# Performance work log

Hardware: AMD Instinct MI355X
Metric: run time of the kernel (lower is better)

## Reference

```python
import jax, jax.numpy as jnp
import numpy as np

D = 48; N_IN = 8192; K = 24; RADIUS = 0.033
C_HID = 86; C_IN = 5; EMB = 16; MODES = 6; PAD = 6; N_LAYERS = 4
EPS = 1e-5


def _pos_embed(x):
    # neuraloperator PositionalEmbedding: scalar -> EMB channels (cos || sin)
    half = EMB // 2
    freqs = (1.0 / 10000.0) ** (jnp.arange(half, dtype=x.dtype) / half)
    ang = x[:, None] * freqs[None, :]
    return jnp.concatenate([jnp.cos(ang), jnp.sin(ang)], axis=-1)


def _gelu(x):
    return jax.nn.gelu(x, approximate=False)


def _conv1x1(h, w, b):
    return jnp.einsum('oi,ixyz->oxyz', w, h) + b[:, None, None, None]


def _group_norm(h, w, b):
    # GroupNorm(num_groups=1) on a batch-1 [C,X,Y,Z] tensor
    mu = jnp.mean(h)
    var = jnp.var(h)
    hn = (h - mu) * jax.lax.rsqrt(var + EPS)
    return hn * w[:, None, None, None] + b[:, None, None, None]


def _spectral_conv(h, wr, wi):
    S = h.shape[1]
    Xf = jnp.fft.rfftn(h, axes=(1, 2, 3))  # [C,S,S,S//2+1] complex64
    W = wr + 1j * wi                        # [4,C,C,m,m,m]
    out = jnp.zeros_like(Xf)
    m = MODES
    sls = (slice(0, m), slice(-m, None))
    c = 0
    for a in range(2):
        for b in range(2):
            blk = Xf[:, sls[a], sls[b], :m]
            res = jnp.einsum('ixyz,ioxyz->oxyz', blk, W[c])
            out = out.at[:, sls[a], sls[b], :m].set(res)
            c += 1
    return jnp.fft.irfftn(out, s=(S, S, S), axes=(1, 2, 3))


def _forward(x_in, x_out, df, w_lift, b_lift, spec_wr, spec_wi,
             w_skip, b_skip, mlp1_w, mlp1_b, mlp2_w, mlp2_b, wms, bms,
             g1_w, g1_b, g2_w, g2_b, k1_w, k1_b, k2_w, k2_b, k3_w, k3_b,
             p1_w, p1_b, p2_w, p2_b, nb_idx, nb_mask):
    n_out = D ** 3
    x_out_embed = _pos_embed(x_out.reshape(-1)).reshape(n_out, 3 * EMB)
    feat = jnp.concatenate([df, jnp.transpose(x_out, (3, 0, 1, 2))], axis=0)  # [5,D,D,D]
    h = _conv1x1(feat, w_lift, b_lift)
    h = jnp.pad(h, ((0, 0), (0, PAD), (0, PAD), (0, PAD)))  # one-sided domain padding
    for l in range(N_LAYERS):
        skip = _conv1x1(h, w_skip[l], b_skip[l])
        hf = _group_norm(_spectral_conv(h, spec_wr[l], spec_wi[l]), g1_w[l], g1_b[l])
        h = hf + skip
        if l < N_LAYERS - 1:
            h = _gelu(h)
        mskip = _conv1x1(h, wms[l], bms[l])
        hm = _conv1x1(_gelu(_conv1x1(h, mlp1_w[l], mlp1_b[l])), mlp2_w[l], mlp2_b[l])
        hm = _group_norm(hm, g2_w[l], g2_b[l])
        h = hm + mskip
        if l < N_LAYERS - 1:
            h = _gelu(h)
    h = h[:, :D, :D, :D]
    f_y = h.reshape(C_HID, n_out).T  # [n_out, C_HID]
    x_in_embed = _pos_embed(x_in.reshape(-1)).reshape(N_IN, 3 * EMB)
    # GNO: gather -> kernel MLP -> elementwise (linear kernel) -> mean scatter-reduce
    y_g = x_out_embed[nb_idx]                                        # [N,K,48]
    q_g = jnp.broadcast_to(x_in_embed[:, None, :], (N_IN, K, 3 * EMB))
    kin = jnp.concatenate([y_g, q_g], axis=-1)                       # [N,K,96]
    k = _gelu(kin @ k1_w.T + k1_b)
    k = _gelu(k @ k2_w.T + k2_b)
    k = k @ k3_w.T + k3_b                                            # [N,K,C_HID]
    f_g = f_y[nb_idx]                                                # [N,K,C_HID]
    mask = nb_mask[..., None].astype(k.dtype)
    num = jnp.sum(k * f_g * mask, axis=1)
    den = jnp.maximum(jnp.sum(nb_mask, axis=1), 1).astype(k.dtype)[:, None]
    out = num / den
    out = _gelu(out @ p1_w.T + p1_b)
    return out @ p2_w.T + p2_b                                       # [N,1]


def setup_inputs():
    rng = np.random.default_rng(0)
    lin = np.linspace(0.0, 1.0, D, dtype=np.float32)
    gx, gy, gz = np.meshgrid(lin, lin, lin, indexing='ij')
    x_out = np.stack([gx, gy, gz], axis=-1)                          # [D,D,D,3]
    x_in = rng.random((N_IN, 3)).astype(np.float32)
    # --- host-side ball-query neighbor search (regular grid, radius=RADIUS) ---
    spacing = 1.0 / (D - 1)
    rc = int(np.ceil(RADIUS / spacing))
    offs = np.arange(-rc, rc + 1)
    oi, oj, ok = np.meshgrid(offs, offs, offs, indexing='ij')
    offsets = np.stack([oi.ravel(), oj.ravel(), ok.ravel()], axis=-1)
    base = np.floor(x_in / spacing + 0.5).astype(np.int64)
    cand = base[:, None, :] + offsets[None, :, :]
    ok_v = np.all((cand >= 0) & (cand < D), axis=-1)
    cand = np.clip(cand, 0, D - 1)
    d2 = np.sum((cand.astype(np.float32) * spacing - x_in[:, None, :]) ** 2, axis=-1)
    inball = ok_v & (d2 <= RADIUS ** 2)
    order = np.argsort(~inball, axis=1, kind='stable')[:, :K]
    flat = (cand[..., 0] * D + cand[..., 1]) * D + cand[..., 2]
    nb_idx = np.take_along_axis(flat, order, axis=1).astype(np.int32)
    nb_mask = np.take_along_axis(inball, order, axis=1)

    def lw(o, i):
        return jnp.asarray((rng.standard_normal((o, i)) / np.sqrt(i)).astype(np.float32))

    def slw(n, o, i):
        return jnp.asarray((rng.standard_normal((n, o, i)) / np.sqrt(i)).astype(np.float32))

    m = MODES
    ss = 1.0 / C_HID
    spec_wr = jnp.asarray((rng.standard_normal((N_LAYERS, 4, C_HID, C_HID, m, m, m)) * ss).astype(np.float32))
    spec_wi = jnp.asarray((rng.standard_normal((N_LAYERS, 4, C_HID, C_HID, m, m, m)) * ss).astype(np.float32))
    zC = jnp.zeros((N_LAYERS, C_HID), dtype=jnp.float32)
    oC = jnp.ones((N_LAYERS, C_HID), dtype=jnp.float32)
    return dict(
        x_in=jnp.asarray(x_in), x_out=jnp.asarray(x_out),
        df=jnp.asarray(rng.standard_normal((C_IN - 3, D, D, D)).astype(np.float32)),
        nb_idx=jnp.asarray(nb_idx), nb_mask=jnp.asarray(nb_mask),
        w_lift=lw(C_HID, C_IN), b_lift=jnp.zeros(C_HID, dtype=jnp.float32),
        spec_wr=spec_wr, spec_wi=spec_wi,
        w_skip=slw(N_LAYERS, C_HID, C_HID), b_skip=zC,
        mlp1_w=slw(N_LAYERS, C_HID, C_HID), mlp1_b=zC,
        mlp2_w=slw(N_LAYERS, C_HID, C_HID), mlp2_b=zC,
        wms=slw(N_LAYERS, C_HID, C_HID), bms=zC,
        g1_w=oC, g1_b=zC, g2_w=oC, g2_b=zC,
        k1_w=lw(512, 6 * EMB), k1_b=jnp.zeros(512, dtype=jnp.float32),
        k2_w=lw(256, 512), k2_b=jnp.zeros(256, dtype=jnp.float32),
        k3_w=lw(C_HID, 256), k3_b=jnp.zeros(C_HID, dtype=jnp.float32),
        p1_w=lw(256, C_HID), p1_b=jnp.zeros(256, dtype=jnp.float32),
        p2_w=lw(1, 256), p2_b=jnp.zeros(1, dtype=jnp.float32),
    )


def reference(x_in, x_out, df, nb_idx, nb_mask, w_lift, b_lift, spec_wr, spec_wi,
              w_skip, b_skip, mlp1_w, mlp1_b, mlp2_w, mlp2_b, wms, bms,
              g1_w, g1_b, g2_w, g2_b, k1_w, k1_b, k2_w, k2_b, k3_w, k3_b,
              p1_w, p1_b, p2_w, p2_b):
    return _forward(x_in, x_out, df, w_lift, b_lift, spec_wr, spec_wi,
                    w_skip, b_skip, mlp1_w, mlp1_b, mlp2_w, mlp2_b, wms, bms,
                    g1_w, g1_b, g2_w, g2_b, k1_w, k1_b, k2_w, k2_b, k3_w, k3_b,
                    p1_w, p1_b, p2_w, p2_b, nb_idx, nb_mask)
```

## Files before the change

kernel.cpp:

```cpp
#include <hip/hip_runtime.h>
#include <math.h>

#define CH 86
#define SP 54
#define SS2 2916
#define SS3 157464
#define DG 48
#define MPAD 157568
#define RT_ROWS (CH*SS2)
#define NSLICE (CH*SP)
#define PI_F 3.14159265358979323846f
#define GN_INV (1.0/13541904.0)

static constexpr size_t A512(size_t x){ return (x + 511) & ~((size_t)511); }
static constexpr size_t HB2 = (size_t)CH*SS3*2;
static constexpr size_t HB4 = (size_t)CH*SS3*4;
static constexpr size_t AB2 = (size_t)MPAD*96*2;
static constexpr size_t XB4 = (size_t)MPAD*96*4;
static constexpr size_t FAB = (size_t)CH*SS2*6*8;
static constexpr size_t FBB = (size_t)CH*SP*12*6*8;
static constexpr size_t FCB = (size_t)CH*864*8;
static constexpr size_t OFF_HA = 0;
static constexpr size_t OFF_HS = OFF_HA + A512(HB2);
static constexpr size_t OFF_AB = OFF_HS + A512(HB4);
static constexpr size_t OFF_BB = OFF_AB + A512(AB2);
static constexpr size_t OFF_XSC= OFF_BB + A512(AB2);
static constexpr size_t OFF_FA = OFF_XSC+ A512(XB4);
static constexpr size_t OFF_FB = OFF_FA + A512(FAB);
static constexpr size_t OFF_FC = OFF_FB + A512(FBB);
static constexpr size_t OFF_FD = OFF_FC + A512(FCB);
static constexpr size_t OFF_FE = OFF_FD + A512(FCB);
static constexpr size_t OFF_ST = OFF_FE + A512(FBB);
static constexpr size_t OFF_WB = OFF_ST + 512;
static constexpr size_t OFF_P1W= OFF_WB + A512((size_t)16*96*96*2);
static constexpr size_t OFF_W1 = OFF_P1W+ A512((size_t)256*96*2);
static constexpr size_t OFF_W2 = OFF_W1 + A512((size_t)512*96*2);
static constexpr size_t OFF_W3 = OFF_W2 + A512((size_t)256*512*2);
static constexpr size_t OFF_K3 = OFF_W3 + A512((size_t)86*256*2);
static constexpr size_t OFF_Z2 = OFF_K3 + A512((size_t)196608*CH*4);
static constexpr size_t OFF_U  = OFF_Z2 + A512((size_t)98304*256*2);
static constexpr size_t OFF_H1 = OFF_U  + A512((size_t)8192*96*2);
static constexpr int    CHUNK_M = 98304;
static constexpr size_t OFF_KIN = 0;
static constexpr size_t OFF_Z1  = A512((size_t)CHUNK_M*96*2);

typedef __attribute__((ext_vector_type(8))) short bf16x8;
typedef __attribute__((ext_vector_type(4))) float f32x4;

__device__ __forceinline__ float gelu_f(float x){
  return 0.5f*x*(1.0f + erff(x*0.70710678118654752440f));
}
__device__ __forceinline__ unsigned short f2bf(float x){
  unsigned u = __float_as_uint(x);
  u += 0x7fffu + ((u>>16)&1u);
  return (unsigned short)(u>>16);
}
__device__ __forceinline__ float bf2f(unsigned short u){
  return __uint_as_float(((unsigned)u)<<16);
}

__global__ void k_zero_stats(double* st){ if (threadIdx.x < 16) st[threadIdx.x] = 0.0; }

__global__ __launch_bounds__(256) void k_f2bf(const float* __restrict__ in,
    unsigned short* __restrict__ out, int n)
{
  int i = blockIdx.x*256 + threadIdx.x;
  if (i < n) out[i] = f2bf(in[i]);
}

__global__ __launch_bounds__(256) void k_wprep(const float* __restrict__ src,
    unsigned short* __restrict__ dst, int slot)
{
  int l = blockIdx.y;
  int idx = blockIdx.x*256 + threadIdx.x;
  int n = idx/96, k = idx-96*n;
  unsigned short v = 0;
  if (n < 86 && k < 86) v = f2bf(src[(size_t)l*7396 + n*86 + k]);
  dst[(size_t)(l*4+slot)*9216 + idx] = v;
}

__global__ __launch_bounds__(256) void k_pad_w(const float* __restrict__ src,
    unsigned short* __restrict__ dst, int rows)
{
  int idx = blockIdx.x*256 + threadIdx.x;
  if (idx >= rows*96) return;
  int n = idx/96, k = idx-96*n;
  dst[idx] = (k<86)? f2bf(src[n*86+k]) : (unsigned short)0;
}

__global__ __launch_bounds__(256) void k_lift(const float* __restrict__ df,
    const float* __restrict__ wl, const float* __restrict__ bl,
    unsigned short* __restrict__ hA, unsigned short* __restrict__ Ab)
{
  __shared__ float vals[128*96];
  const int t = threadIdx.x;
  const int s0 = blockIdx.x*128;
  for(int idx=t; idx<128*96; idx+=256){
    int sl = idx/96, o = idx-96*sl;
    int s = s0+sl;
    float v = 0.f;
    if (o < 86){
      int x = s/2916, r2 = s-2916*x, y = r2/54, z = r2-54*y;
      if (x<DG && y<DG && z<DG){
        int p = (x*DG + y)*DG + z;
        v = wl[o*5]*df[p] + wl[o*5+1]*df[110592+p]
          + wl[o*5+2]*(x*(1.0f/47.0f)) + wl[o*5+3]*(y*(1.0f/47.0f))
          + wl[o*5+4]*(z*(1.0f/47.0f)) + bl[o];
      }
    }
    vals[idx] = v;
  }
  __syncthreads();
  for(int idx=t; idx<128*96; idx+=256)
    Ab[(size_t)s0*96 + idx] = f2bf(vals[idx]);
  for(int idx=t; idx<86*128; idx+=256){
    int c = idx/128, sl = idx-128*c;
    int s = s0+sl;
    if (s < SS3) hA[(size_t)c*SS3 + s] = f2bf(vals[sl*96 + c]);
  }
}

__global__ __launch_bounds__(256) void k_dft_z(const unsigned short* __restrict__ h, float* __restrict__ A)
{
  __shared__ alignas(16) float rows[64*55];
  __shared__ float twc[6*54], tws[6*54];
  const int t = threadIdx.x;
  for(int idx=t; idx<6*54; idx+=256){
    int k = idx/54, z = idx-54*k;
    int m = (k*z)%54;
    float ang = -(2.0f*PI_F/54.0f)*(float)m;
    twc[idx]=cosf(ang); tws[idx]=sinf(ang);
  }
  const int r0 = blockIdx.x*64;
  for(int idx=t; idx<64*54; idx+=256){
    int r = idx/54;
    rows[r*55 + (idx-54*r)] = (r0+r < RT_ROWS)? bf2f(h[(size_t)r0*54 + idx]) : 0.f;
  }
  __syncthreads();
  for(int oi=t; oi<768; oi+=256){
    int r = oi & 63;
    int k = (oi>>6)%6;
    int part = oi/384;
    if (r0+r < RT_ROWS){
      const float* tw = part? tws : twc;
      const float* rp = &rows[r*55];
      const float* twk = &tw[k*54];
      float acc=0.f;
      #pragma unroll 6
      for(int z=0;z<54;z++) acc += rp[z]*twk[z];
      A[((size_t)(r0+r)*6 + k)*2 + part] = acc;
    }
  }
}

__global__ __launch_bounds__(256) void k_dft_y(const float* __restrict__ A, float* __restrict__ B)
{
  __shared__ float asl[4*648];
  __shared__ float twc[12*54], tws[12*54];
  const int t = threadIdx.x;
  for(int idx=t; idx<12*54; idx+=256){
    int kyi = idx/54, y = idx-54*kyi;
    int ky = (kyi<6)? kyi : (42+kyi);
    int m = (ky*y)%54;
    float ang = -(2.0f*PI_F/54.0f)*(float)m;
    twc[idx]=cosf(ang); tws[idx]=sinf(ang);
  }
  const int s0 = blockIdx.x*4;
  for(int idx=t; idx<4*648; idx+=256){
    int sl = idx/648;
    asl[idx] = (s0+sl < NSLICE)? A[(size_t)s0*648 + idx] : 0.f;
  }
  __syncthreads();
  for(int oi=t; oi<4*72; oi+=256){
    int sl = oi/72, o = oi-72*sl;
    if (s0+sl >= NSLICE) continue;
    int kyi = o/6, kz = o-6*kyi;
    const float* base = &asl[sl*648];
    float cr=0.f, ci=0.f;
    for(int y=0;y<54;y++){
      float ar = base[(y*6+kz)*2], ai = base[(y*6+kz)*2+1];
      float tc = twc[kyi*54+y], ts = tws[kyi*54+y];
      cr += ar*tc - ai*ts;
      ci += ar*ts + ai*tc;
    }
    size_t ob = ((size_t)(s0+sl)*12 + kyi)*6 + kz;
    B[ob*2]=cr; B[ob*2+1]=ci;
  }
}

__global__ __launch_bounds__(256) void k_dft_x(const float* __restrict__ B, float* __restrict__ C)
{
  __shared__ float bsl[7776];
  __shared__ float twc[12*54], tws[12*54];
  const int t = threadIdx.x;
  const int i = blockIdx.x;
  for(int idx=t; idx<12*54; idx+=256){
    int kxi = idx/54, x = idx-54*kxi;
    int kx = (kxi<6)? kxi : (42+kxi);
    int m = (kx*x)%54;
    float ang = -(2.0f*PI_F/54.0f)*(float)m;
    twc[idx]=cosf(ang); tws[idx]=sinf(ang);
  }
  for(int idx=t; idx<7776; idx+=256) bsl[idx] = B[(size_t)i*7776 + idx];
  __syncthreads();
  for(int oi=t; oi<864; oi+=256){
    int kxi = oi/72, rest = oi-72*kxi;
    float cr=0.f, ci=0.f;
    for(int x=0;x<54;x++){
      float br = bsl[(x*72+rest)*2], bi = bsl[(x*72+rest)*2+1];
      float tc = twc[kxi*54+x], ts = tws[kxi*54+x];
      cr += br*tc - bi*ts;
      ci += br*ts + bi*tc;
    }
    int kyi = rest/6, kz = rest-6*kyi;
    int c = ((kxi>=6)?2:0) + ((kyi>=6)?1:0);
    int f = ((kxi%6)*6 + (kyi%6))*6 + kz;
    size_t ob = ((size_t)i*4 + c)*216 + f;
    C[ob*2]=cr; C[ob*2+1]=ci;
  }
}

__global__ __launch_bounds__(256) void k_mix(const float* __restrict__ C,
    const float* __restrict__ wr, const float* __restrict__ wi, float* __restrict__ D)
{
  const int f = threadIdx.x;
  if (f >= 216) return;
  const int o = blockIdx.x, c = blockIdx.y;
  const size_t wstride = (size_t)CH*216;
  const float* wrp = wr + ((size_t)c*CH*CH + o)*216 + f;
  const float* wip = wi + ((size_t)c*CH*CH + o)*216 + f;
  const float* cp  = C + ((size_t)c*216 + f)*2;
  float ar=0.f, ai=0.f;
  #pragma unroll 4
  for(int i=0;i<CH;i++){
    float cr = cp[0], cim = cp[1];
    float xr = *wrp, xi = *wip;
    ar += cr*xr - cim*xi;
    ai += cr*xi + cim*xr;
    wrp += wstride; wip += wstride;
    cp += 864*2;
  }
  int mx = f/36, my = (f/6)%6, kz = f%6;
  int kxi = mx + ((c>=2)?6:0);
  int kyi = my + ((c&1)?6:0);
  size_t ob = (((size_t)o*12 + kxi)*12 + kyi)*6 + kz;
  D[ob*2]=ar; D[ob*2+1]=ai;
}

__global__ __launch_bounds__(256) void k_idft_x(const float* __restrict__ D, float* __restrict__ E)
{
  __shared__ float dsl[1728];
  __shared__ float twc[12*54], tws[12*54];
  const int t = threadIdx.x;
  const int o = blockIdx.x;
  for(int idx=t; idx<12*54; idx+=256){
    int kxi = idx/54, x = idx-54*kxi;
    int kx = (kxi<6)? kxi : (42+kxi);
    int m = (kx*x)%54;
    float ang = (2.0f*PI_F/54.0f)*(float)m;
    twc[idx]=cosf(ang); tws[idx]=sinf(ang);
  }
  for(int idx=t; idx<1728; idx+=256) dsl[idx] = D[(size_t)o*1728 + idx];
  __syncthreads();
  for(int oi=t; oi<3888; oi+=256){
    int x = oi/72, rest = oi-72*x;
    float er=0.f, ei=0.f;
    #pragma unroll
    for(int kxi=0;kxi<12;kxi++){
      float dr = dsl[(kxi*72+rest)*2], di = dsl[(kxi*72+rest)*2+1];
      float tc = twc[kxi*54+x], ts = tws[kxi*54+x];
      er += dr*tc - di*ts;
      ei += dr*ts + di*tc;
    }
    size_t ob = (size_t)o*3888 + oi;
    E[ob*2]=er; E[ob*2+1]=ei;
  }
}

__global__ __launch_bounds__(256) void k_idft_y(const float* __restrict__ E, float* __restrict__ F)
{
  __shared__ float esl[4*144];
  __shared__ float twc[12*54], tws[12*54];
  const int t = threadIdx.x;
  for(int idx=t; idx<12*54; idx+=256){
    int kyi = idx/54, y = idx-54*kyi;
    int ky = (kyi<6)? kyi : (42+kyi);
    int m = (ky*y)%54;
    float ang = (2.0f*PI_F/54.0f)*(float)m;
    twc[idx]=cosf(ang); tws[idx]=sinf(ang);
  }
  const int s0 = blockIdx.x*4;
  for(int idx=t; idx<4*144; idx+=256){
    int sl = idx/144;
    esl[idx] = (s0+sl < NSLICE)? E[(size_t)s0*144 + idx] : 0.f;
  }
  __syncthreads();
  for(int oi=t; oi<4*324; oi+=256){
    int sl = oi/324, rest = oi-324*sl;
    if (s0+sl >= NSLICE) continue;
    int y = rest/6, kz = rest-6*y;
    const float* base = &esl[sl*144];
    float fr=0.f, fi=0.f;
    #pragma unroll
    for(int kyi=0;kyi<12;kyi++){
      float er = base[(kyi*6+kz)*2], ei = base[(kyi*6+kz)*2+1];
      float tc = twc[kyi*54+y], ts = tws[kyi*54+y];
      fr += er*tc - ei*ts;
      fi += er*ts + ei*tc;
    }
    size_t ob = ((size_t)(s0+sl)*54 + y)*6 + kz;
    F[ob*2]=fr; F[ob*2+1]=fi;
  }
}

__global__ __launch_bounds__(256) void k_idft_z(const float* __restrict__ F,
    float* __restrict__ hs, double* __restrict__ st)
{
  __shared__ float rws[64*12];
  __shared__ float twc[5*54], tws[5*54];
  __shared__ float red[8];
  const int t = threadIdx.x;
  for(int idx=t; idx<5*54; idx+=256){
    int k = idx/54 + 1, z = idx%54;
    int m = (k*z)%54;
    float ang = (2.0f*PI_F/54.0f)*(float)m;
    twc[idx]=cosf(ang); tws[idx]=sinf(ang);
  }
  const int r0 = blockIdx.x*64;
  for(int idx=t; idx<768; idx+=256){
    int r = idx/12;
    rws[idx] = (r0+r < RT_ROWS)? F[(size_t)r0*12 + idx] : 0.f;
  }
  __syncthreads();
  const float inv = 1.0f/157464.0f;
  float lsum=0.f, lsq=0.f;
  for(int oi=t; oi<64*54; oi+=256){
    int r = oi/54, z = oi-54*r;
    if (r0+r < RT_ROWS){
      const float* fr = &rws[r*12];
      float acc = fr[0];
      #pragma unroll
      for(int k=1;k<=5;k++)
        acc += 2.0f*(fr[2*k]*twc[(k-1)*54+z] - fr[2*k+1]*tws[(k-1)*54+z]);
      acc *= inv;
      hs[(size_t)r0*54 + oi] = acc;
      lsum += acc; lsq += acc*acc;
    }
  }
  #pragma unroll
  for(int off=32; off; off>>=1){
    lsum += __shfl_down(lsum, off, 64);
    lsq  += __shfl_down(lsq,  off, 64);
  }
  if ((t&63)==0){ red[(t>>6)*2]=lsum; red[(t>>6)*2+1]=lsq; }
  __syncthreads();
  if (t==0){
    double s1 = (double)red[0]+red[2]+red[4]+red[6];
    double s2 = (double)red[1]+red[3]+red[5]+red[7];
    atomicAdd(st, s1); atomicAdd(st+1, s2);
  }
}

template<int ACT1>
__global__ __launch_bounds__(256) void k_fuse3(
    const unsigned short* __restrict__ Ain, const unsigned short* __restrict__ Wl3,
    const float* __restrict__ bsk, const float* __restrict__ b1,
    const float* __restrict__ b2,
    const float* __restrict__ hS, const float* __restrict__ g1,
    const float* __restrict__ bg1, const double* __restrict__ st1,
    double* __restrict__ st2,
    unsigned short* __restrict__ Bb, float* __restrict__ Hm)
{
  __shared__ unsigned short Wl[96*96];
  __shared__ unsigned short Achunk[8*512];
  __shared__ unsigned short Tt[128*96];
  __shared__ float red[8];
  const int t = threadIdx.x, lane = t&63, w = t>>6;
  const int m0 = blockIdx.x*128;
  const int lr = lane>>2, lq = lane&3;
  const int colb = lane&15, rowq = (lane>>4)*4;
  f32x4 acc[2][6];

  for(int s=w; s<18; s+=4){
    const unsigned short* gw = Wl3 + s*512 + lane*8;
    __builtin_amdgcn_global_load_lds((const __attribute__((address_space(1))) void*)gw,
        (__attribute__((address_space(3))) void*)&Wl[s*512], 16, 0, 0);
  }
  #pragma unroll
  for(int s=0;s<2;s++)
    #pragma unroll
    for(int n=0;n<6;n++) acc[s][n] = (f32x4){0.f,0.f,0.f,0.f};
  #pragma unroll
  for(int k0=0;k0<96;k0+=32){
    __syncthreads();
    #pragma unroll
    for(int j=0;j<2;j++){
      int slot = w*2+j;
      int row = slot*16 + lr;
      const unsigned short* ga = Ain + (size_t)(m0+row)*96 + k0 + lq*8;
      __builtin_amdgcn_global_load_lds((const __attribute__((address_space(1))) void*)ga,
          (__attribute__((address_space(3))) void*)&Achunk[slot*512], 16, 0, 0);
    }
    __syncthreads();
    bf16x8 af[2], bf[6];
    #pragma unroll
    for(int s=0;s<2;s++)
      af[s] = *(const bf16x8*)&Achunk[(w*32 + s*16 + (lane&15))*32 + (lane>>4)*8];
    #pragma unroll
    for(int n=0;n<6;n++)
      bf[n] = *(const bf16x8*)&Wl[(n*16 + (lane&15))*96 + k0 + (lane>>4)*8];
    #pragma unroll
    for(int s=0;s<2;s++)
      #pragma unroll
      for(int n=0;n<6;n++)
        acc[s][n] = __builtin_amdgcn_mfma_f32_16x16x32_bf16(af[s], bf[n], acc[s][n], 0, 0, 0);
  }
  {
    double m = st1[0]*GN_INV;
    double va = st1[1]*GN_INV - m*m;
    float mu = (float)m, rs = (float)(1.0/sqrt(va + 1e-5));
    #pragma unroll
    for(int n=0;n<6;n++){
      int col = n*16 + colb;
      bool cv = (col < CH);
      float bn=0.f, gg=1.f, bb=0.f;
      if (cv){ bn = bsk[col]; gg = g1[col]; bb = bg1[col]; }
      #pragma unroll
      for(int s=0;s<2;s++){
        #pragma unroll
        for(int r=0;r<4;r++){
          int rowl = w*32 + s*16 + rowq + r;
          int row = m0 + rowl;
          float v = 0.f;
          if (cv){
            v = acc[s][n][r] + bn;
            if (row < SS3) v += (hS[(size_t)col*SS3 + row]-mu)*rs*gg + bb;
            if (ACT1) v = gelu_f(v);
          }
          unsigned short vb = f2bf(v);
          Bb[(size_t)row*96 + col] = vb;
          Tt[rowl*96 + col] = vb;
        }
      }
    }
  }

  __syncthreads();
  for(int s=w; s<18; s+=4){
    const unsigned short* gw = Wl3 + 9216 + s*512 + lane*8;
    __builtin_amdgcn_global_load_lds((const __attribute__((address_space(1))) void*)gw,
        (__attribute__((address_space(3))) void*)&Wl[s*512], 16, 0, 0);
  }
  #pragma unroll
  for(int s=0;s<2;s++)
    #pragma unroll
    for(int n=0;n<6;n++) acc[s][n] = (f32x4){0.f,0.f,0.f,0.f};
  __syncthreads();
  #pragma unroll
  for(int k0=0;k0<96;k0+=32){
    bf16x8 af[2], bf[6];
    #pragma unroll
    for(int s=0;s<2;s++)
      af[s] = *(const bf16x8*)&Tt[(w*32 + s*16 + (lane&15))*96 + k0 + (lane>>4)*8];
    #pragma unroll
    for(int n=0;n<6;n++)
      bf[n] = *(const bf16x8*)&Wl[(n*16 + (lane&15))*96 + k0 + (lane>>4)*8];
    #pragma unroll
    for(int s=0;s<2;s++)
      #pragma unroll
      for(int n=0;n<6;n++)
        acc[s][n] = __builtin_amdgcn_mfma_f32_16x16x32_bf16(af[s], bf[n], acc[s][n], 0, 0, 0);
  }
  #pragma unroll
  for(int n=0;n<6;n++){
    int col = n*16 + colb;
    bool cv = (col < CH);
    float bn = cv? b1[col] : 0.f;
    #pragma unroll
    for(int s=0;s<2;s++){
      #pragma unroll
      for(int r=0;r<4;r++){
        int rowl = w*32 + s*16 + rowq + r;
        float v = cv? gelu_f(acc[s][n][r] + bn) : 0.f;
        Tt[rowl*96 + col] = f2bf(v);
      }
    }
  }

  __syncthreads();
  for(int s=w; s<18; s+=4){
    const unsigned short* gw = Wl3 + 18432 + s*512 + lane*8;
    __builtin_amdgcn_global_load_lds((const __attribute__((address_space(1))) void*)gw,
        (__attribute__((address_space(3))) void*)&Wl[s*512], 16, 0, 0);
  }
  #pragma unroll
  for(int s=0;s<2;s++)
    #pragma unroll
    for(int n=0;n<6;n++) acc[s][n] = (f32x4){0.f,0.f,0.f,0.f};
  __syncthreads();
  #pragma unroll
  for(int k0=0;k0<96;k0+=32){
    bf16x8 af[2], bf[6];
    #pragma unroll
    for(int s=0;s<2;s++)
      af[s] = *(const bf16x8*)&Tt[(w*32 + s*16 + (lane&15))*96 + k0 + (lane>>4)*8];
    #pragma unroll
    for(int n=0;n<6;n++)
      bf[n] = *(const bf16x8*)&Wl[(n*16 + (lane&15))*96 + k0 + (lane>>4)*8];
    #pragma unroll
    for(int s=0;s<2;s++)
      #pragma unroll
      for(int n=0;n<6;n++)
        acc[s][n] = __builtin_amdgcn_mfma_f32_16x16x32_bf16(af[s], bf[n], acc[s][n], 0, 0, 0);
  }
  float lsum=0.f, lsq=0.f;
  #pragma unroll
  for(int n=0;n<6;n++){
    int col = n*16 + colb;
    bool cv = (col < CH);
    float bn = cv? b2[col] : 0.f;
    #pragma unroll
    for(int s=0;s<2;s++){
      #pragma unroll
      for(int r=0;r<4;r++){
        int row = m0 + w*32 + s*16 + rowq + r;
        float v = 0.f;
        if (cv){
          v = acc[s][n][r] + bn;
          if (row < SS3){ lsum += v; lsq += v*v; }
        }
        Hm[(size_t)row*96 + col] = v;
      }
    }
  }
  #pragma unroll
  for(int off=32; off; off>>=1){
    lsum += __shfl_down(lsum, off, 64);
    lsq  += __shfl_down(lsq,  off, 64);
  }
  if (lane==0){ red[w*2]=lsum; red[w*2+1]=lsq; }
  __syncthreads();
  if (t==0){
    double s1 = (double)red[0]+red[2]+red[4]+red[6];
    double s2 = (double)red[1]+red[3]+red[5]+red[7];
    atomicAdd(st2, s1); atomicAdd(st2+1, s2);
  }
}

template<int LAST>
__global__ __launch_bounds__(256) void k_convms(
    const unsigned short* __restrict__ Ain, const unsigned short* __restrict__ Wm,
    const float* __restrict__ bms,
    const float* __restrict__ Hm, const float* __restrict__ g2,
    const float* __restrict__ bg2, const double* __restrict__ st2,
    unsigned short* __restrict__ Ab, unsigned short* __restrict__ hA,
    float* __restrict__ FY)
{
  __shared__ unsigned short Wl[96*96];
  __shared__ unsigned short Achunk[8*512];
  const int t = threadIdx.x, lane = t&63, w = t>>6;
  const int m0 = blockIdx.x*128;
  const int lr = lane>>2, lq = lane&3;
  for(int s=w; s<18; s+=4){
    const unsigned short* gw = Wm + s*512 + lane*8;
    __builtin_amdgcn_global_load_lds((const __attribute__((address_space(1))) void*)gw,
        (__attribute__((address_space(3))) void*)&Wl[s*512], 16, 0, 0);
  }
  f32x4 acc[2][6];
  #pragma unroll
  for(int s=0;s<2;s++)
    #pragma unroll
    for(int n=0;n<6;n++) acc[s][n] = (f32x4){0.f,0.f,0.f,0.f};
  #pragma unroll
  for(int k0=0;k0<96;k0+=32){
    __syncthreads();
    #pragma unroll
    for(int j=0;j<2;j++){
      int slot = w*2+j;
      int row = slot*16 + lr;
      const unsigned short* ga = Ain + (size_t)(m0+row)*96 + k0 + lq*8;
      __builtin_amdgcn_global_load_lds((const __attribute__((address_space(1))) void*)ga,
          (__attribute__((address_space(3))) void*)&Achunk[slot*512], 16, 0, 0);
    }
    __syncthreads();
    bf16x8 af[2], bf[6];
    #pragma unroll
    for(int s=0;s<2;s++)
      af[s] = *(const bf16x8*)&Achunk[(w*32 + s*16 + (lane&15))*32 + (lane>>4)*8];
    #pragma unroll
    for(int n=0;n<6;n++)
      bf[n] = *(const bf16x8*)&Wl[(n*16 + (lane&15))*96 + k0 + (lane>>4)*8];
    #pragma unroll
    for(int s=0;s<2;s++)
      #pragma unroll
      for(int n=0;n<6;n++)
        acc[s][n] = __builtin_amdgcn_mfma_f32_16x16x32_bf16(af[s], bf[n], acc[s][n], 0, 0, 0);
  }
  double m = st2[0]*GN_INV;
  double va = st2[1]*GN_INV - m*m;
  float mu = (float)m, rs = (float)(1.0/sqrt(va + 1e-5));
  const int colb = lane&15, rowq = (lane>>4)*4;
  #pragma unroll
  for(int n=0;n<6;n++){
    int col = n*16 + colb;
    bool cv = (col < CH);
    float bn=0.f, gg=1.f, bb=0.f;
    if (cv){ bn = bms[col]; gg = g2[col]; bb = bg2[col]; }
    #pragma unroll
    for(int s=0;s<2;s++){
      #pragma unroll
      for(int r=0;r<4;r++){
        int row = m0 + w*32 + s*16 + rowq + r;
        float v = 0.f;
        if (cv){
          v = acc[s][n][r] + bn + (Hm[(size_t)row*96 + col]-mu)*rs*gg + bb;
          if (!LAST) v = gelu_f(v);
        }
        if (LAST){
          FY[(size_t)row*96 + col] = v;
        } else {
          Ab[(size_t)row*96 + col] = f2bf(v);
          if (cv && row < SS3) hA[(size_t)col*SS3 + row] = f2bf(v);
        }
      }
    }
  }
}

__global__ __launch_bounds__(256) void k_build_kin(const float* __restrict__ x_in,
    const int* __restrict__ nb_idx, unsigned short* __restrict__ kin, int pair0)
{
  int gidx = blockIdx.x*256 + threadIdx.x;
  int lp = gidx/96, col = gidx - lp*96;
  int pair = pair0 + lp;
  int qi = pair/24;
  int cc = col; bool isq = false;
  if (cc >= 48){ cc -= 48; isq = true; }
  int ci = cc>>4, e = cc&15;
  int f = e&7; bool is_sin = (e>=8);
  float coord;
  if (isq){
    coord = x_in[qi*3 + ci];
  } else {
    int pt = nb_idx[pair];
    int gcoord;
    if (ci==0) gcoord = pt/2304;
    else if (ci==1) gcoord = (pt/48)%48;
    else gcoord = pt%48;
    coord = gcoord*(1.0f/47.0f);
  }
  float freq = exp2f(-(float)f * 1.66096404744368117f);
  float ang = coord*freq;
  kin[gidx] = f2bf(is_sin ? sinf(ang) : cosf(ang));
}

template<int ACT, int OUT_BF16>
__global__ __launch_bounds__(256,2) void k_gemm_mfma(
    const unsigned short* __restrict__ A, const unsigned short* __restrict__ B,
    const float* __restrict__ bias, void* __restrict__ Cout,
    int M, int N, int K)
{
  __shared__ unsigned short As[128*32];
  __shared__ unsigned short Bs[128*32];
  const int t = threadIdx.x;
  const int lane = t & 63, w = t >> 6;
  const int wm = w >> 1, wn = w & 1;
  const int m0 = blockIdx.x*128, n0 = blockIdx.y*128;
  const int lr = lane >> 2, lq = lane & 3;
  f32x4 acc[4][4];
  #pragma unroll
  for(int s=0;s<4;s++)
    #pragma unroll
    for(int n=0;n<4;n++) acc[s][n] = (f32x4){0.f,0.f,0.f,0.f};

  for(int k0=0;k0<K;k0+=32){
    __syncthreads();
    #pragma unroll
    for(int j=0;j<2;j++){
      int slot = w*2 + j;
      int row = slot*16 + lr;
      const unsigned short* ga = A + (size_t)(m0+row)*K + k0 + lq*8;
      __builtin_amdgcn_global_load_lds((const __attribute__((address_space(1))) void*)ga,
          (__attribute__((address_space(3))) void*)&As[slot*512], 16, 0, 0);
      int brow = n0 + row; if (brow > N-1) brow = N-1;
      const unsigned short* gb = B + (size_t)brow*K + k0 + lq*8;
      __builtin_amdgcn_global_load_lds((const __attribute__((address_space(1))) void*)gb,
          (__attribute__((address_space(3))) void*)&Bs[slot*512], 16, 0, 0);
    }
    __syncthreads();
    bf16x8 af[4], bg[4];
    #pragma unroll
    for(int s=0;s<4;s++)
      af[s] = *(const bf16x8*)&As[(wm*64 + s*16 + (lane&15))*32 + (lane>>4)*8];
    #pragma unroll
    for(int n=0;n<4;n++)
      bg[n] = *(const bf16x8*)&Bs[(wn*64 + n*16 + (lane&15))*32 + (lane>>4)*8];
    #pragma unroll
    for(int s=0;s<4;s++)
      #pragma unroll
      for(int n=0;n<4;n++)
        acc[s][n] = __builtin_amdgcn_mfma_f32_16x16x32_bf16(af[s], bg[n], acc[s][n], 0, 0, 0);
  }

  unsigned short* Cb = (unsigned short*)Cout;
  float* Cf = (float*)Cout;
  const int colb = n0 + wn*64 + (lane&15);
  const int rowb = m0 + wm*64 + (lane>>4)*4;
  #pragma unroll
  for(int n=0;n<4;n++){
    int col = colb + n*16;
    if (col < N){
      float bn = bias[col];
      #pragma unroll
      for(int s=0;s<4;s++){
        int row = rowb + s*16;
        #pragma unroll
        for(int r=0;r<4;r++){
          float v = acc[s][n][r] + bn;
          if (ACT) v = gelu_f(v);
          if (OUT_BF16) Cb[(size_t)(row+r)*N + col] = f2bf(v);
          else          Cf[(size_t)(row+r)*N + col] = v;
        }
      }
    }
  }
}

__global__ __launch_bounds__(256) void k_gno_u(
    const float* __restrict__ K3, const float* __restrict__ FY,
    const int* __restrict__ nb_idx, const int* __restrict__ nb_mask,
    unsigned short* __restrict__ U)
{
  __shared__ int sidx[4][24];
  __shared__ float smk[4][24];
  const int t = threadIdx.x, w = t>>6, lane = t&63;
  const int i0 = blockIdx.x*4;
  if (t < 96){
    int q = t/24, k = t-24*q;
    int pt = nb_idx[(i0+q)*24+k];
    int x = pt/2304, rem = pt-2304*x, y = rem/48, z = rem-48*y;
    sidx[q][k] = x*2916 + y*54 + z;
    smk[q][k] = (nb_mask[(i0+q)*24+k] != 0)? 1.f : 0.f;
  }
  __syncthreads();
  const int i = i0 + w;
  const int c1 = lane, c2 = 64+lane;
  float a1=0.f, a2=0.f, den=0.f;
  for(int k=0;k<24;k++){
    float mk = smk[w][k];
    den += mk;
    if (mk > 0.f){
      const float* k3p = K3 + (size_t)(i*24+k)*CH;
      const float* fyp = FY + (size_t)sidx[w][k]*96;
      a1 += k3p[c1]*fyp[c1];
      if (c2 < CH) a2 += k3p[c2]*fyp[c2];
    }
  }
  if (den < 1.f) den = 1.f;
  U[(size_t)i*96 + c1] = f2bf(a1/den);
  if (c2 < 96) U[(size_t)i*96 + c2] = f2bf((c2 < CH)? a2/den : 0.f);
}

__global__ __launch_bounds__(256) void k_out(const unsigned short* __restrict__ H1,
    const float* __restrict__ p2w, const float* __restrict__ p2b,
    float* __restrict__ out)
{
  const int t = threadIdx.x, w = t>>6, lane = t&63;
  const int i = blockIdx.x*4 + w;
  const unsigned short* hp = H1 + (size_t)i*256 + lane*4;
  float s = 0.f;
  #pragma unroll
  for(int j=0;j<4;j++) s += bf2f(hp[j]) * p2w[lane*4+j];
  #pragma unroll
  for(int off=32; off; off>>=1) s += __shfl_down(s, off, 64);
  if (lane==0) out[i] = s + p2b[0];
}

extern "C" void kernel_launch(void* const* d_in, const int* in_sizes, int n_in,
                              void* d_out, int out_size, void* d_ws, size_t ws_size,
                              hipStream_t stream)
{
  (void)in_sizes; (void)n_in; (void)out_size; (void)ws_size;
  const float* x_in  = (const float*)d_in[0];
  const float* df    = (const float*)d_in[2];
  const int*   nbidx = (const int*)d_in[3];
  const int*   nbmsk = (const int*)d_in[4];
  const float* wlift = (const float*)d_in[5];
  const float* blift = (const float*)d_in[6];
  const float* spwr  = (const float*)d_in[7];
  const float* spwi  = (const float*)d_in[8];
  const float* wskip = (const float*)d_in[9];
  const float* bskip = (const float*)d_in[10];
  const float* m1w   = (const float*)d_in[11];
  const float* m1b   = (const float*)d_in[12];
  const float* m2w   = (const float*)d_in[13];
  const float* m2b   = (const float*)d_in[14];
  const float* wms   = (const float*)d_in[15];
  const float* bms   = (const float*)d_in[16];
  const float* g1w   = (const float*)d_in[17];
  const float* g1b   = (const float*)d_in[18];
  const float* g2w   = (const float*)d_in[19];
  const float* g2b   = (const float*)d_in[20];
  const float* k1w   = (const float*)d_in[21];
  const float* k1b   = (const float*)d_in[22];
  const float* k2w   = (const float*)d_in[23];
  const float* k2b   = (const float*)d_in[24];
  const float* k3w   = (const float*)d_in[25];
  const float* k3b   = (const float*)d_in[26];
  const float* p1w   = (const float*)d_in[27];
  const float* p1b   = (const float*)d_in[28];
  const float* p2w   = (const float*)d_in[29];
  const float* p2b   = (const float*)d_in[30];
  float* out = (float*)d_out;
  char* ws = (char*)d_ws;

  unsigned short* hAb = (unsigned short*)(ws + OFF_HA);
  float* hS = (float*)(ws + OFF_HS);
  unsigned short* Ab = (unsigned short*)(ws + OFF_AB);
  unsigned short* Bb = (unsigned short*)(ws + OFF_BB);
  float* Xsc = (float*)(ws + OFF_XSC);
  float* fA = (float*)(ws + OFF_FA);
  float* fB = (float*)(ws + OFF_FB);
  float* fC = (float*)(ws + OFF_FC);
  float* fD = (float*)(ws + OFF_FD);
  float* fE = (float*)(ws + OFF_FE);
  double* st= (double*)(ws + OFF_ST);
  unsigned short* Wb = (unsigned short*)(ws + OFF_WB);
  unsigned short* p1wb = (unsigned short*)(ws + OFF_P1W);
  unsigned short* w1b  = (unsigned short*)(ws + OFF_W1);
  unsigned short* w2b  = (unsigned short*)(ws + OFF_W2);
  unsigned short* w3b  = (unsigned short*)(ws + OFF_W3);
  float* K3 = (float*)(ws + OFF_K3);
  unsigned short* Z2b  = (unsigned short*)(ws + OFF_Z2);
  unsigned short* Ub   = (unsigned short*)(ws + OFF_U);
  unsigned short* H1b  = (unsigned short*)(ws + OFF_H1);
  unsigned short* kinb = (unsigned short*)(ws + OFF_KIN);
  unsigned short* Z1b  = (unsigned short*)(ws + OFF_Z1);

  k_zero_stats<<<1,64,0,stream>>>(st);
  k_wprep<<<dim3(36,4),256,0,stream>>>(wskip, Wb, 0);
  k_wprep<<<dim3(36,4),256,0,stream>>>(m1w,   Wb, 1);
  k_wprep<<<dim3(36,4),256,0,stream>>>(m2w,   Wb, 2);
  k_wprep<<<dim3(36,4),256,0,stream>>>(wms,   Wb, 3);
  k_pad_w<<<96,256,0,stream>>>(p1w, p1wb, 256);
  k_f2bf<<<(512*96+255)/256,256,0,stream>>>(k1w, w1b, 512*96);
  k_f2bf<<<(256*512+255)/256,256,0,stream>>>(k2w, w2b, 256*512);
  k_f2bf<<<(86*256+255)/256,256,0,stream>>>(k3w, w3b, 86*256);
  k_lift<<<1231,256,0,stream>>>(df, wlift, blift, hAb, Ab);

  for(int l=0;l<4;l++){
    const float* wr_l = spwr + (size_t)l*4*CH*CH*216;
    const float* wi_l = spwi + (size_t)l*4*CH*CH*216;
    double* st1 = st + l*4;
    double* st2 = st + l*4 + 2;
    k_dft_z<<<3919,256,0,stream>>>(hAb, fA);
    k_dft_y<<<1161,256,0,stream>>>(fA, fB);
    k_dft_x<<<86,256,0,stream>>>(fB, fC);
    k_mix<<<dim3(86,4),256,0,stream>>>(fC, wr_l, wi_l, fD);
    k_idft_x<<<86,256,0,stream>>>(fD, fE);
    k_idft_y<<<1161,256,0,stream>>>(fE, fA);
    k_idft_z<<<3919,256,0,stream>>>(fA, hS, st1);
    const unsigned short* Wl3 = Wb + (size_t)l*4*9216;
    const unsigned short* Wms = Wb + (size_t)(l*4+3)*9216;
    if (l<3){
      k_fuse3<1><<<1231,256,0,stream>>>(Ab, Wl3, bskip+l*86, m1b+l*86, m2b+l*86,
          hS, g1w+l*86, g1b+l*86, st1, st2, Bb, Xsc);
      k_convms<0><<<1231,256,0,stream>>>(Bb, Wms, bms+l*86, Xsc, g2w+l*86, g2b+l*86,
          st2, Ab, hAb, nullptr);
    } else {
      k_fuse3<0><<<1231,256,0,stream>>>(Ab, Wl3, bskip+l*86, m1b+l*86, m2b+l*86,
          hS, g1w+l*86, g1b+l*86, st1, st2, Bb, Xsc);
      k_convms<1><<<1231,256,0,stream>>>(Bb, Wms, bms+l*86, Xsc, g2w+l*86, g2b+l*86,
          st2, nullptr, nullptr, Xsc);
    }
  }

  for(int ch=0; ch<2; ch++){
    int pair0 = ch*CHUNK_M;
    k_build_kin<<<(CHUNK_M*96)/256,256,0,stream>>>(x_in, nbidx, kinb, pair0);
    k_gemm_mfma<1,1><<<dim3(CHUNK_M/128,4),256,0,stream>>>(kinb, w1b, k1b, (void*)Z1b, CHUNK_M, 512, 96);
    k_gemm_mfma<1,1><<<dim3(CHUNK_M/128,2),256,0,stream>>>(Z1b, w2b, k2b, (void*)Z2b, CHUNK_M, 256, 512);
    k_gemm_mfma<0,0><<<dim3(CHUNK_M/128,1),256,0,stream>>>(Z2b, w3b, k3b, (void*)(K3 + (size_t)pair0*CH), CHUNK_M, 86, 256);
  }

  k_gno_u<<<2048,256,0,stream>>>(K3, Xsc, nbidx, nbmsk, Ub);
  k_gemm_mfma<1,1><<<dim3(64,2),256,0,stream>>>(Ub, p1wb, p1b, (void*)H1b, 8192, 256, 96);
  k_out<<<2048,256,0,stream>>>(H1b, p2w, p2b, out);
}
```

Before: 2.205 ms.

## Stage spectral output as bf16 row-major and stage tile writes through LDS

A new transpose kernel converts the channel-major fp32 spectral output into a row-major bf16 buffer so k_fuse3 can read it coalesced, instead of making strided per-element reads from hS. k_fuse3 and k_convms now load A fragments straight into registers, use padded LDS tiles, and write Bb, Ab and the channel-major hA through LDS with vectorized coalesced stores. k_gemm_mfma also reads A directly from global memory and drops its 2-blocks-per-CU launch bound. The cost is one extra kernel launch per layer plus a buffer round trip, and the spectral residual is now rounded to bf16 before the group norm, which lowers precision.

```diff
diff --git a/kernel.cpp b/kernel.cpp
--- a/kernel.cpp
+++ b/kernel.cpp
@@ -40,6 +40,7 @@
 static constexpr size_t OFF_Z2 = OFF_K3 + A512((size_t)196608*CH*4);
 static constexpr size_t OFF_U  = OFF_Z2 + A512((size_t)98304*256*2);
 static constexpr size_t OFF_H1 = OFF_U  + A512((size_t)8192*96*2);
+static constexpr size_t OFF_HT = OFF_K3;
 static constexpr int    CHUNK_M = 98304;
 static constexpr size_t OFF_KIN = 0;
 static constexpr size_t OFF_Z1  = A512((size_t)CHUNK_M*96*2);
@@ -361,59 +362,82 @@
   }
 }
 
+__global__ __launch_bounds__(256) void k_tr(const float* __restrict__ hS,
+    unsigned short* __restrict__ hT)
+{
+  __shared__ float tile[128*101];
+  const int t = threadIdx.x;
+  const int s0 = blockIdx.x*128;
+  for(int idx=t; idx<86*128; idx+=256){
+    int c = idx>>7, sl = idx&127;
+    int s = s0+sl;
+    tile[sl*101+c] = (s<SS3)? hS[(size_t)c*SS3+s] : 0.f;
+  }
+  for(int idx=t; idx<128*10; idx+=256){
+    int sl = idx/10, c = 86 + idx%10;
+    tile[sl*101+c] = 0.f;
+  }
+  __syncthreads();
+  for(int idx=t; idx<1536; idx+=256){
+    int r = idx/12, g = idx-12*r;
+    bf16x8 o;
+    #pragma unroll
+    for(int j=0;j<8;j++) o[j] = (short)f2bf(tile[r*101+g*8+j]);
+    *(bf16x8*)&hT[(size_t)(s0+r)*96 + g*8] = o;
+  }
+}
+
 template<int ACT1>
 __global__ __launch_bounds__(256) void k_fuse3(
     const unsigned short* __restrict__ Ain, const unsigned short* __restrict__ Wl3,
     const float* __restrict__ bsk, const float* __restrict__ b1,
     const float* __restrict__ b2,
-    const float* __restrict__ hS, const float* __restrict__ g1,
+    const unsigned short* __restrict__ hT, const float* __restrict__ g1,
     const float* __restrict__ bg1, const double* __restrict__ st1,
     double* __restrict__ st2,
     unsigned short* __restrict__ Bb, float* __restrict__ Hm)
 {
-  __shared__ unsigned short Wl[96*96];
-  __shared__ unsigned short Achunk[8*512];
-  __shared__ unsigned short Tt[128*96];
+  __shared__ alignas(16) unsigned short Wl[96*104];
+  __shared__ alignas(16) unsigned short T[128*104];
   __shared__ float red[8];
   const int t = threadIdx.x, lane = t&63, w = t>>6;
   const int m0 = blockIdx.x*128;
-  const int lr = lane>>2, lq = lane&3;
-  const int colb = lane&15, rowq = (lane>>4)*4;
+  const int colb = lane&15, rowq = (lane>>4)*4, half = lane>>4;
   f32x4 acc[2][6];
 
-  for(int s=w; s<18; s+=4){
-    const unsigned short* gw = Wl3 + s*512 + lane*8;
-    __builtin_amdgcn_global_load_lds((const __attribute__((address_space(1))) void*)gw,
-        (__attribute__((address_space(3))) void*)&Wl[s*512], 16, 0, 0);
+  for(int idx=t; idx<1152; idx+=256){
+    int r = idx/12, g = idx-12*r;
+    *(bf16x8*)&Wl[r*104+g*8] = *(const bf16x8*)&Wl3[r*96+g*8];
+  }
+  for(int idx=t; idx<1536; idx+=256){
+    int r = idx/12, g = idx-12*r;
+    *(bf16x8*)&T[r*104+g*8] = *(const bf16x8*)&hT[(size_t)(m0+r)*96 + g*8];
+  }
+  bf16x8 afr[2][3];
+  {
+    const unsigned short* Abase = Ain + (size_t)(m0 + w*32 + colb)*96 + half*8;
+    #pragma unroll
+    for(int s=0;s<2;s++)
+      #pragma unroll
+      for(int q=0;q<3;q++)
+        afr[s][q] = *(const bf16x8*)(Abase + s*16*96 + q*32);
   }
   #pragma unroll
   for(int s=0;s<2;s++)
     #pragma unroll
     for(int n=0;n<6;n++) acc[s][n] = (f32x4){0.f,0.f,0.f,0.f};
-  #pragma unroll
-  for(int k0=0;k0<96;k0+=32){
-    __syncthreads();
-    #pragma unroll
-    for(int j=0;j<2;j++){
-      int slot = w*2+j;
-      int row = slot*16 + lr;
-      const unsigned short* ga = Ain + (size_t)(m0+row)*96 + k0 + lq*8;
-      __builtin_amdgcn_global_load_lds((const __attribute__((address_space(1))) void*)ga,
-          (__attribute__((address_space(3))) void*)&Achunk[slot*512], 16, 0, 0);
-    }
-    __syncthreads();
-    bf16x8 af[2], bf[6];
+  __syncthreads();
+  #pragma unroll
+  for(int q=0;q<3;q++){
+    bf16x8 bf[6];
+    #pragma unroll
+    for(int n=0;n<6;n++)
+      bf[n] = *(const bf16x8*)&Wl[(n*16+colb)*104 + q*32 + half*8];
     #pragma unroll
     for(int s=0;s<2;s++)
-      af[s] = *(const bf16x8*)&Achunk[(w*32 + s*16 + (lane&15))*32 + (lane>>4)*8];
-    #pragma unroll
-    for(int n=0;n<6;n++)
-      bf[n] = *(const bf16x8*)&Wl[(n*16 + (lane&15))*96 + k0 + (lane>>4)*8];
-    #pragma unroll
-    for(int s=0;s<2;s++)
       #pragma unroll
       for(int n=0;n<6;n++)
-        acc[s][n] = __builtin_amdgcn_mfma_f32_16x16x32_bf16(af[s], bf[n], acc[s][n], 0, 0, 0);
+        acc[s][n] = __builtin_amdgcn_mfma_f32_16x16x32_bf16(afr[s][q], bf[n], acc[s][n], 0, 0, 0);
   }
   {
     double m = st1[0]*GN_INV;
@@ -430,46 +454,44 @@
         #pragma unroll
         for(int r=0;r<4;r++){
           int rowl = w*32 + s*16 + rowq + r;
-          int row = m0 + rowl;
           float v = 0.f;
           if (cv){
-            v = acc[s][n][r] + bn;
-            if (row < SS3) v += (hS[(size_t)col*SS3 + row]-mu)*rs*gg + bb;
+            v = acc[s][n][r] + bn + (bf2f(T[rowl*104+col])-mu)*rs*gg + bb;
             if (ACT1) v = gelu_f(v);
           }
-          unsigned short vb = f2bf(v);
-          Bb[(size_t)row*96 + col] = vb;
-          Tt[rowl*96 + col] = vb;
+          T[rowl*104+col] = f2bf(v);
         }
       }
     }
   }
-
-  __syncthreads();
-  for(int s=w; s<18; s+=4){
-    const unsigned short* gw = Wl3 + 9216 + s*512 + lane*8;
-    __builtin_amdgcn_global_load_lds((const __attribute__((address_space(1))) void*)gw,
-        (__attribute__((address_space(3))) void*)&Wl[s*512], 16, 0, 0);
-  }
+  __syncthreads();
+  for(int idx=t; idx<1536; idx+=256){
+    int r = idx/12, g = idx-12*r;
+    *(bf16x8*)&Bb[(size_t)(m0+r)*96 + g*8] = *(const bf16x8*)&T[r*104+g*8];
+  }
+  for(int idx=t; idx<1152; idx+=256){
+    int r = idx/12, g = idx-12*r;
+    *(bf16x8*)&Wl[r*104+g*8] = *(const bf16x8*)&Wl3[9216 + r*96+g*8];
+  }
+  __syncthreads();
   #pragma unroll
   for(int s=0;s<2;s++)
     #pragma unroll
     for(int n=0;n<6;n++) acc[s][n] = (f32x4){0.f,0.f,0.f,0.f};
-  __syncthreads();
-  #pragma unroll
-  for(int k0=0;k0<96;k0+=32){
-    bf16x8 af[2], bf[6];
+  #pragma unroll
+  for(int q=0;q<3;q++){
+    bf16x8 a2[2], bf[6];
     #pragma unroll
     for(int s=0;s<2;s++)
-      af[s] = *(const bf16x8*)&Tt[(w*32 + s*16 + (lane&15))*96 + k0 + (lane>>4)*8];
+      a2[s] = *(const bf16x8*)&T[(w*32+s*16+colb)*104 + q*32 + half*8];
     #pragma unroll
     for(int n=0;n<6;n++)
-      bf[n] = *(const bf16x8*)&Wl[(n*16 + (lane&15))*96 + k0 + (lane>>4)*8];
+      bf[n] = *(const bf16x8*)&Wl[(n*16+colb)*104 + q*32 + half*8];
     #pragma unroll
     for(int s=0;s<2;s++)
       #pragma unroll
       for(int n=0;n<6;n++)
-        acc[s][n] = __builtin_amdgcn_mfma_f32_16x16x32_bf16(af[s], bf[n], acc[s][n], 0, 0, 0);
+        acc[s][n] = __builtin_amdgcn_mfma_f32_16x16x32_bf16(a2[s], bf[n], acc[s][n], 0, 0, 0);
   }
   #pragma unroll
   for(int n=0;n<6;n++){
@@ -482,36 +504,34 @@
       for(int r=0;r<4;r++){
         int rowl = w*32 + s*16 + rowq + r;
         float v = cv? gelu_f(acc[s][n][r] + bn) : 0.f;
-        Tt[rowl*96 + col] = f2bf(v);
+        T[rowl*104+col] = f2bf(v);
       }
     }
   }
-
-  __syncthreads();
-  for(int s=w; s<18; s+=4){
-    const unsigned short* gw = Wl3 + 18432 + s*512 + lane*8;
-    __builtin_amdgcn_global_load_lds((const __attribute__((address_space(1))) void*)gw,
-        (__attribute__((address_space(3))) void*)&Wl[s*512], 16, 0, 0);
-  }
+  __syncthreads();
+  for(int idx=t; idx<1152; idx+=256){
+    int r = idx/12, g = idx-12*r;
+    *(bf16x8*)&Wl[r*104+g*8] = *(const bf16x8*)&Wl3[18432 + r*96+g*8];
+  }
+  __syncthreads();
   #pragma unroll
   for(int s=0;s<2;s++)
     #pragma unroll
     for(int n=0;n<6;n++) acc[s][n] = (f32x4){0.f,0.f,0.f,0.f};
-  __syncthreads();
-  #pragma unroll
-  for(int k0=0;k0<96;k0+=32){
-    bf16x8 af[2], bf[6];
+  #pragma unroll
+  for(int q=0;q<3;q++){
+    bf16x8 a2[2], bf[6];
     #pragma unroll
     for(int s=0;s<2;s++)
-      af[s] = *(const bf16x8*)&Tt[(w*32 + s*16 + (lane&15))*96 + k0 + (lane>>4)*8];
+      a2[s] = *(const bf16x8*)&T[(w*32+s*16+colb)*104 + q*32 + half*8];
     #pragma unroll
     for(int n=0;n<6;n++)
-      bf[n] = *(const bf16x8*)&Wl[(n*16 + (lane&15))*96 + k0 + (lane>>4)*8];
+      bf[n] = *(const bf16x8*)&Wl[(n*16+colb)*104 + q*32 + half*8];
     #pragma unroll
     for(int s=0;s<2;s++)
       #pragma unroll
       for(int n=0;n<6;n++)
-        acc[s][n] = __builtin_amdgcn_mfma_f32_16x16x32_bf16(af[s], bf[n], acc[s][n], 0, 0, 0);
+        acc[s][n] = __builtin_amdgcn_mfma_f32_16x16x32_bf16(a2[s], bf[n], acc[s][n], 0, 0, 0);
   }
   float lsum=0.f, lsq=0.f;
   #pragma unroll
@@ -556,50 +576,45 @@
     unsigned short* __restrict__ Ab, unsigned short* __restrict__ hA,
     float* __restrict__ FY)
 {
-  __shared__ unsigned short Wl[96*96];
-  __shared__ unsigned short Achunk[8*512];
+  __shared__ alignas(16) unsigned short Wl[96*104];
+  __shared__ alignas(16) unsigned short T[128*104];
   const int t = threadIdx.x, lane = t&63, w = t>>6;
   const int m0 = blockIdx.x*128;
-  const int lr = lane>>2, lq = lane&3;
-  for(int s=w; s<18; s+=4){
-    const unsigned short* gw = Wm + s*512 + lane*8;
-    __builtin_amdgcn_global_load_lds((const __attribute__((address_space(1))) void*)gw,
-        (__attribute__((address_space(3))) void*)&Wl[s*512], 16, 0, 0);
+  const int colb = lane&15, rowq = (lane>>4)*4, half = lane>>4;
+  for(int idx=t; idx<1152; idx+=256){
+    int r = idx/12, g = idx-12*r;
+    *(bf16x8*)&Wl[r*104+g*8] = *(const bf16x8*)&Wm[r*96+g*8];
+  }
+  bf16x8 afr[2][3];
+  {
+    const unsigned short* Abase = Ain + (size_t)(m0 + w*32 + colb)*96 + half*8;
+    #pragma unroll
+    for(int s=0;s<2;s++)
+      #pragma unroll
+      for(int q=0;q<3;q++)
+        afr[s][q] = *(const bf16x8*)(Abase + s*16*96 + q*32);
   }
   f32x4 acc[2][6];
   #pragma unroll
   for(int s=0;s<2;s++)
     #pragma unroll
     for(int n=0;n<6;n++) acc[s][n] = (f32x4){0.f,0.f,0.f,0.f};
-  #pragma unroll
-  for(int k0=0;k0<96;k0+=32){
-    __syncthreads();
-    #pragma unroll
-    for(int j=0;j<2;j++){
-      int slot = w*2+j;
-      int row = slot*16 + lr;
-      const unsigned short* ga = Ain + (size_t)(m0+row)*96 + k0 + lq*8;
-      __builtin_amdgcn_global_load_lds((const __attribute__((address_space(1))) void*)ga,
-          (__attribute__((address_space(3))) void*)&Achunk[slot*512], 16, 0, 0);
-    }
-    __syncthreads();
-    bf16x8 af[2], bf[6];
+  __syncthreads();
+  #pragma unroll
+  for(int q=0;q<3;q++){
+    bf16x8 bf[6];
+    #pragma unroll
+    for(int n=0;n<6;n++)
+      bf[n] = *(const bf16x8*)&Wl[(n*16+colb)*104 + q*32 + half*8];
     #pragma unroll
     for(int s=0;s<2;s++)
-      af[s] = *(const bf16x8*)&Achunk[(w*32 + s*16 + (lane&15))*32 + (lane>>4)*8];
-    #pragma unroll
-    for(int n=0;n<6;n++)
-      bf[n] = *(const bf16x8*)&Wl[(n*16 + (lane&15))*96 + k0 + (lane>>4)*8];
-    #pragma unroll
-    for(int s=0;s<2;s++)
       #pragma unroll
       for(int n=0;n<6;n++)
-        acc[s][n] = __builtin_amdgcn_mfma_f32_16x16x32_bf16(af[s], bf[n], acc[s][n], 0, 0, 0);
+        acc[s][n] = __builtin_amdgcn_mfma_f32_16x16x32_bf16(afr[s][q], bf[n], acc[s][n], 0, 0, 0);
   }
   double m = st2[0]*GN_INV;
   double va = st2[1]*GN_INV - m*m;
   float mu = (float)m, rs = (float)(1.0/sqrt(va + 1e-5));
-  const int colb = lane&15, rowq = (lane>>4)*4;
   #pragma unroll
   for(int n=0;n<6;n++){
     int col = n*16 + colb;
@@ -610,18 +625,30 @@
     for(int s=0;s<2;s++){
       #pragma unroll
       for(int r=0;r<4;r++){
-        int row = m0 + w*32 + s*16 + rowq + r;
+        int rowl = w*32 + s*16 + rowq + r;
+        int row = m0 + rowl;
         float v = 0.f;
         if (cv){
           v = acc[s][n][r] + bn + (Hm[(size_t)row*96 + col]-mu)*rs*gg + bb;
           if (!LAST) v = gelu_f(v);
         }
-        if (LAST){
-          FY[(size_t)row*96 + col] = v;
-        } else {
-          Ab[(size_t)row*96 + col] = f2bf(v);
-          if (cv && row < SS3) hA[(size_t)col*SS3 + row] = f2bf(v);
-        }
+        if (LAST) FY[(size_t)row*96 + col] = v;
+        else      T[rowl*104+col] = f2bf(v);
+      }
+    }
+  }
+  if (!LAST){
+    __syncthreads();
+    for(int idx=t; idx<1536; idx+=256){
+      int r = idx/12, g = idx-12*r;
+      *(bf16x8*)&Ab[(size_t)(m0+r)*96 + g*8] = *(const bf16x8*)&T[r*104+g*8];
+    }
+    for(int idx=t; idx<86*64; idx+=256){
+      int c = idx>>6, p = idx&63;
+      int s = m0 + 2*p;
+      if (s < SS3){
+        unsigned v2 = (unsigned)T[(2*p)*104+c] | ((unsigned)T[(2*p+1)*104+c] << 16);
+        *(unsigned*)(hA + (size_t)c*SS3 + s) = v2;
       }
     }
   }
@@ -655,12 +682,11 @@
 }
 
 template<int ACT, int OUT_BF16>
-__global__ __launch_bounds__(256,2) void k_gemm_mfma(
+__global__ __launch_bounds__(256) void k_gemm_mfma(
     const unsigned short* __restrict__ A, const unsigned short* __restrict__ B,
     const float* __restrict__ bias, void* __restrict__ Cout,
     int M, int N, int K)
 {
-  __shared__ unsigned short As[128*32];
   __shared__ unsigned short Bs[128*32];
   const int t = threadIdx.x;
   const int lane = t & 63, w = t >> 6;
@@ -672,6 +698,7 @@
   for(int s=0;s<4;s++)
     #pragma unroll
     for(int n=0;n<4;n++) acc[s][n] = (f32x4){0.f,0.f,0.f,0.f};
+  const unsigned short* Abase = A + (size_t)(m0 + wm*64 + (lane&15))*K + (lane>>4)*8;
 
   for(int k0=0;k0<K;k0+=32){
     __syncthreads();
@@ -679,19 +706,17 @@
     for(int j=0;j<2;j++){
       int slot = w*2 + j;
       int row = slot*16 + lr;
-      const unsigned short* ga = A + (size_t)(m0+row)*K + k0 + lq*8;
-      __builtin_amdgcn_global_load_lds((const __attribute__((address_space(1))) void*)ga,
-          (__attribute__((address_space(3))) void*)&As[slot*512], 16, 0, 0);
       int brow = n0 + row; if (brow > N-1) brow = N-1;
       const unsigned short* gb = B + (size_t)brow*K + k0 + lq*8;
       __builtin_amdgcn_global_load_lds((const __attribute__((address_space(1))) void*)gb,
           (__attribute__((address_space(3))) void*)&Bs[slot*512], 16, 0, 0);
     }
+    bf16x8 af[4];
+    #pragma unroll
+    for(int s=0;s<4;s++)
+      af[s] = *(const bf16x8*)(Abase + (size_t)s*16*K + k0);
     __syncthreads();
-    bf16x8 af[4], bg[4];
-    #pragma unroll
-    for(int s=0;s<4;s++)
-      af[s] = *(const bf16x8*)&As[(wm*64 + s*16 + (lane&15))*32 + (lane>>4)*8];
+    bf16x8 bg[4];
     #pragma unroll
     for(int n=0;n<4;n++)
       bg[n] = *(const bf16x8*)&Bs[(wn*64 + n*16 + (lane&15))*32 + (lane>>4)*8];
@@ -831,6 +856,7 @@
   unsigned short* w2b  = (unsigned short*)(ws + OFF_W2);
   unsigned short* w3b  = (unsigned short*)(ws + OFF_W3);
   float* K3 = (float*)(ws + OFF_K3);
+  unsigned short* hT = (unsigned short*)(ws + OFF_HT);
   unsigned short* Z2b  = (unsigned short*)(ws + OFF_Z2);
   unsigned short* Ub   = (unsigned short*)(ws + OFF_U);
   unsigned short* H1b  = (unsigned short*)(ws + OFF_H1);
@@ -860,16 +886,17 @@
     k_idft_x<<<86,256,0,stream>>>(fD, fE);
     k_idft_y<<<1161,256,0,stream>>>(fE, fA);
     k_idft_z<<<3919,256,0,stream>>>(fA, hS, st1);
+    k_tr<<<1231,256,0,stream>>>(hS, hT);
     const unsigned short* Wl3 = Wb + (size_t)l*4*9216;
     const unsigned short* Wms = Wb + (size_t)(l*4+3)*9216;
     if (l<3){
       k_fuse3<1><<<1231,256,0,stream>>>(Ab, Wl3, bskip+l*86, m1b+l*86, m2b+l*86,
-          hS, g1w+l*86, g1b+l*86, st1, st2, Bb, Xsc);
+          hT, g1w+l*86, g1b+l*86, st1, st2, Bb, Xsc);
       k_convms<0><<<1231,256,0,stream>>>(Bb, Wms, bms+l*86, Xsc, g2w+l*86, g2b+l*86,
           st2, Ab, hAb, nullptr);
     } else {
       k_fuse3<0><<<1231,256,0,stream>>>(Ab, Wl3, bskip+l*86, m1b+l*86, m2b+l*86,
-          hS, g1w+l*86, g1b+l*86, st1, st2, Bb, Xsc);
+          hT, g1w+l*86, g1b+l*86, st1, st2, Bb, Xsc);
       k_convms<1><<<1231,256,0,stream>>>(Bb, Wms, bms+l*86, Xsc, g2w+l*86, g2b+l*86,
           st2, nullptr, nullptr, Xsc);
     }
```

Measured after the change: 2.294 ms. 1.04x slower.
